# Kernel tuning notes

Hardware: AMD Instinct MI355X
Metric: run time of the kernel (lower is better)

## Reference

```python
import jax, jax.numpy as jnp
import numpy as np

# ---- static config (matches init_kwargs) ----
B, L, C = 32, 512, 32
PRED = 96
D = 256
PS, STRIDE = 16, 8
P = (L - PS) // STRIDE + 1  # 63 patches
H = 4
DH = D // H                 # 64 per head
K = 4                        # causal conv kernel size
NB = 2                       # num sLSTM blocks
UP = 384                     # round_up(1.3 * 256, 64) gated-FFN inner dim


def setup_inputs() -> dict:
    key = jax.random.key(0)
    ks = iter(jax.random.split(key, 32))
    def nrm(shape, s=0.02):
        return jax.random.normal(next(ks), shape, dtype=jnp.float32) * s
    f32 = jnp.float32
    return dict(
        x=jax.random.normal(next(ks), (B, L, C), dtype=f32),
        W_emb=nrm((PS, D)), b_emb=jnp.zeros((D,), f32),
        ln1_w=jnp.ones((NB, D), f32), ln1_b=jnp.zeros((NB, D), f32),
        conv_w=nrm((NB, K, D), 0.1), conv_b=jnp.zeros((NB, D), f32),
        Wg=nrm((NB, 4, H, DH, DH), 0.05),   # input gate projections (i,f,z,o), block-diag per head
        Rg=nrm((NB, 4, H, DH, DH), 0.05),   # recurrent kernels per head
        gb=jnp.zeros((NB, 4, D), f32),      # gate biases
        gn_w=jnp.ones((NB, D), f32),        # per-head groupnorm weight
        ln2_w=jnp.ones((NB, D), f32), ln2_b=jnp.zeros((NB, D), f32),
        up_w=nrm((NB, D, 2 * UP)), up_b=jnp.zeros((NB, 2 * UP), f32),
        dn_w=nrm((NB, UP, D)), dn_b=jnp.zeros((NB, D), f32),
        post_w=jnp.ones((D,), f32), post_b=jnp.zeros((D,), f32),
        W_proj=nrm((D * P, PRED)), b_proj=jnp.zeros((PRED,), f32),
    )


def _layernorm(x, w, b, eps=1e-5):
    mu = x.mean(-1, keepdims=True)
    var = x.var(-1, keepdims=True)
    return (x - mu) / jnp.sqrt(var + eps) * w + b


def _slstm_layer(x, conv_w, conv_b, Wg, Rg, gb, gn_w):
    # x: (N, S, D)
    N, S, _ = x.shape
    # causal depthwise conv (k=K) + swish -> feeds i,f gates
    xp = jnp.pad(x, ((0, 0), (K - 1, 0), (0, 0)))
    xc = sum(xp[:, k:k + S, :] * conv_w[k] for k in range(K)) + conv_b
    xc = xc * jax.nn.sigmoid(xc)
    xh = x.reshape(N, S, H, DH)
    xch = xc.reshape(N, S, H, DH)
    gi = jnp.einsum('nshd,hde->nshe', xch, Wg[0]) + gb[0].reshape(H, DH)
    gf = jnp.einsum('nshd,hde->nshe', xch, Wg[1]) + gb[1].reshape(H, DH)
    gz = jnp.einsum('nshd,hde->nshe', xh, Wg[2]) + gb[2].reshape(H, DH)
    go = jnp.einsum('nshd,hde->nshe', xh, Wg[3]) + gb[3].reshape(H, DH)
    gates = jnp.moveaxis(jnp.stack([gi, gf, gz, go], 0), 2, 0)  # (S, 4, N, H, DH)

    def step(carry, g):
        c, n, h, m = carry  # each (N, H, DH)
        rec = jnp.einsum('nhd,ghde->gnhe', h, Rg)  # (4, N, H, DH)
        ip, fp, zp, op = g[0] + rec[0], g[1] + rec[1], g[2] + rec[2], g[3] + rec[3]
        logf = m + jax.nn.log_sigmoid(fp)          # log(f_t) + m_{t-1}
        m_new = jnp.maximum(ip, logf)              # stabilizer
        i = jnp.exp(ip - m_new)
        f = jnp.exp(logf - m_new)
        c_new = f * c + i * jnp.tanh(zp)
        n_new = f * n + i
        h_new = jax.nn.sigmoid(op) * c_new / n_new
        return (c_new, n_new, h_new, m_new), h_new

    z0 = jnp.zeros((N, H, DH), x.dtype)
    _, hs = jax.lax.scan(step, (z0, z0, z0, z0), gates)
    y = jnp.moveaxis(hs, 0, 1)  # (N, S, H, DH)
    mu = y.mean(-1, keepdims=True)
    var = y.var(-1, keepdims=True)
    y = (y - mu) / jnp.sqrt(var + 1e-5)            # per-head groupnorm
    return y.reshape(N, S, D) * gn_w


def reference(x, W_emb, b_emb, ln1_w, ln1_b, conv_w, conv_b, Wg, Rg, gb, gn_w,
              ln2_w, ln2_b, up_w, up_b, dn_w, dn_b, post_w, post_b, W_proj, b_proj):
    Bb, Ll, Cc = x.shape
    xs = x.transpose(0, 2, 1).reshape(Bb * Cc, Ll)              # (N, L)
    idx = np.arange(P)[:, None] * STRIDE + np.arange(PS)[None, :]
    patches = xs[:, idx]                                         # (N, P, PS) unfold
    h = patches @ W_emb + b_emb                                  # (N, P, D)
    for blk in range(NB):
        h = h + _slstm_layer(_layernorm(h, ln1_w[blk], ln1_b[blk]),
                             conv_w[blk], conv_b[blk], Wg[blk], Rg[blk], gb[blk], gn_w[blk])
        u = _layernorm(h, ln2_w[blk], ln2_b[blk]) @ up_w[blk] + up_b[blk]
        g1, g2 = jnp.split(u, 2, axis=-1)
        h = h + (jax.nn.gelu(g1) * g2) @ dn_w[blk] + dn_b[blk]   # gated FFN
    h = _layernorm(h, post_w, post_b)                            # post-blocks norm
    out = h.reshape(Bb * Cc, D * P) @ W_proj + b_proj            # (N, PRED)
    return out.reshape(Bb, Cc, PRED).transpose(0, 2, 1)          # (B, PRED, C)
```

## Files before the change

### kernel.cpp

```cpp
#include <hip/hip_runtime.h>
#include <stdint.h>

typedef unsigned short u16;
typedef unsigned int   u32;
typedef __attribute__((ext_vector_type(8))) short bf16x8;
typedef __attribute__((ext_vector_type(4))) float f32x4;

#define NS      63
#define NSEQ    1024
#define DDIM    256
#define NHEAD   4
#define DHEAD   64
#define UPDIM   384
#define PREDN   96
#define LLEN    512
#define CCH     32
#define PSIZE   16
#define PSTRIDE 8
#define KC_PROJ 8
#define KCHUNK_PROJ 2016

__device__ __forceinline__ float bf2f(u32 lo16){
  union { u32 i; float f; } v; v.i = lo16 << 16; return v.f;
}
__device__ __forceinline__ float bf2f_hi(u32 u){
  union { u32 i; float f; } v; v.i = u & 0xffff0000u; return v.f;
}
__device__ __forceinline__ u16 f2bf(float f){
  union { u32 i; float f; } v; v.f = f;
  u32 u = v.i; u += 0x7fffu + ((u >> 16) & 1u);
  return (u16)(u >> 16);
}

__device__ __forceinline__ void gload16(const u16* g, u16* lds){
  __builtin_amdgcn_global_load_lds(
      (const __attribute__((address_space(1))) u32*)g,
      (__attribute__((address_space(3))) u32*)lds, 16, 0, 0);
}

template<int N> __device__ __forceinline__ void waitcnt_vm(){
  if constexpr (N == 0) asm volatile("s_waitcnt vmcnt(0)" ::: "memory");
  else if constexpr (N == 4) asm volatile("s_waitcnt vmcnt(4)" ::: "memory");
  else if constexpr (N == 6) asm volatile("s_waitcnt vmcnt(6)" ::: "memory");
}

__global__ __launch_bounds__(256) void cvt_transpose_t(
    const float* __restrict__ src, u16* __restrict__ dst, int R, int C){
  __shared__ u16 tile[32][33];
  int rb = blockIdx.x*32, cb = blockIdx.y*32;
  int tx = threadIdx.x & 31, ty = threadIdx.x >> 5;
  #pragma unroll
  for (int i = ty; i < 32; i += 8){
    int r = rb + i, c = cb + tx;
    tile[i][tx] = (r < R && c < C) ? f2bf(src[(size_t)r*C + c]) : (u16)0;
  }
  __syncthreads();
  #pragma unroll
  for (int i = ty; i < 32; i += 8){
    int c = cb + i, r = rb + tx;
    if (c < C && r < R) dst[(size_t)c*R + r] = tile[tx][i];
  }
}

__global__ __launch_bounds__(256) void cvt_gate(
    const float* __restrict__ src, u16* __restrict__ dst){
  int mat = blockIdx.x, t = threadIdx.x;
  const float* s = src + (size_t)mat*4096;
  u16* d = dst + (size_t)mat*4096;
  for (int i = t; i < 4096; i += 256){
    int r = i >> 6, c = i & 63;
    d[c*64 + r] = f2bf(s[i]);
  }
}

__global__ __launch_bounds__(256) void cvt_gateW2(
    const float* __restrict__ Wg, u16* __restrict__ dst){
  int mi = blockIdx.x;
  int blk = mi >> 3, p = (mi >> 2) & 1, hd = mi & 3;
  u16* d = dst + (size_t)mi*8192;
  for (int i = threadIdx.x; i < 8192; i += 256){
    int n = i >> 6, k = i & 63;
    int e = n >> 1, gl = n & 1;
    int g = 2*p + gl;
    d[i] = f2bf(Wg[((((size_t)blk*4 + g)*4 + hd)*64 + k)*64 + e]);
  }
}

__global__ __launch_bounds__(256) void patch_embed_ln_v(
    const float* __restrict__ x, const float* __restrict__ Wemb,
    const float* __restrict__ bemb, const float* __restrict__ w1,
    const float* __restrict__ b1, u16* __restrict__ h,
    u16* __restrict__ outA, int t_base){
  int wv = blockIdx.x*4 + (threadIdx.x >> 6);
  int lane = threadIdx.x & 63;
  int tg = t_base + wv;
  int n = tg / NS, s = tg - n*NS;
  int b = n >> 5, c = n & 31;
  int l0 = s * PSTRIDE;
  float4 acc = *(const float4*)(bemb + lane*4);
  #pragma unroll
  for (int p = 0; p < PSIZE; ++p){
    float xv = x[((size_t)b*LLEN + l0 + p)*CCH + c];
    float4 we = *(const float4*)(Wemb + p*DDIM + lane*4);
    acc.x += xv*we.x; acc.y += xv*we.y; acc.z += xv*we.z; acc.w += xv*we.w;
  }
  ushort4 hu; hu.x=f2bf(acc.x); hu.y=f2bf(acc.y); hu.z=f2bf(acc.z); hu.w=f2bf(acc.w);
  *(ushort4*)(h + (size_t)wv*DDIM + lane*4) = hu;
  float s1 = acc.x+acc.y+acc.z+acc.w;
  float s2 = acc.x*acc.x+acc.y*acc.y+acc.z*acc.z+acc.w*acc.w;
  #pragma unroll
  for (int o = 1; o < 64; o <<= 1){ s1 += __shfl_xor(s1,o,64); s2 += __shfl_xor(s2,o,64); }
  float mu = s1*(1.f/DDIM);
  float var = s2*(1.f/DDIM) - mu*mu;
  float rstd = rsqrtf(var + 1e-5f);
  float4 wf = *(const float4*)(w1 + lane*4);
  float4 bf = *(const float4*)(b1 + lane*4);
  ushort4 o4;
  o4.x = f2bf((acc.x-mu)*rstd*wf.x + bf.x);
  o4.y = f2bf((acc.y-mu)*rstd*wf.y + bf.y);
  o4.z = f2bf((acc.z-mu)*rstd*wf.z + bf.z);
  o4.w = f2bf((acc.w-mu)*rstd*wf.w + bf.w);
  *(ushort4*)(outA + (size_t)wv*DDIM + lane*4) = o4;
}

__global__ __launch_bounds__(256) void layernorm_v(
    const u16* __restrict__ in, const float* __restrict__ w,
    const float* __restrict__ b, u16* __restrict__ out){
  int wv = blockIdx.x*4 + (threadIdx.x >> 6);
  int lane = threadIdx.x & 63;
  ushort4 u = *(const ushort4*)(in + (size_t)wv*DDIM + lane*4);
  float v0=bf2f(u.x), v1=bf2f(u.y), v2=bf2f(u.z), v3=bf2f(u.w);
  float s1 = v0+v1+v2+v3, s2 = v0*v0+v1*v1+v2*v2+v3*v3;
  #pragma unroll
  for (int o = 1; o < 64; o <<= 1){ s1 += __shfl_xor(s1,o,64); s2 += __shfl_xor(s2,o,64); }
  float mu = s1*(1.f/DDIM);
  float var = s2*(1.f/DDIM) - mu*mu;
  float rstd = rsqrtf(var + 1e-5f);
  float4 wf = *(const float4*)(w + lane*4);
  float4 bf = *(const float4*)(b + lane*4);
  ushort4 o4;
  o4.x = f2bf((v0-mu)*rstd*wf.x + bf.x);
  o4.y = f2bf((v1-mu)*rstd*wf.y + bf.y);
  o4.z = f2bf((v2-mu)*rstd*wf.z + bf.z);
  o4.w = f2bf((v3-mu)*rstd*wf.w + bf.w);
  *(ushort4*)(out + (size_t)wv*DDIM + lane*4) = o4;
}

__global__ __launch_bounds__(256) void gn_res_ln_v(
    const u16* __restrict__ y, const float* __restrict__ gnw,
    const float* __restrict__ w2, const float* __restrict__ b2,
    u16* __restrict__ h, u16* __restrict__ outA){
  int wv = blockIdx.x*4 + (threadIdx.x >> 6);
  int lane = threadIdx.x & 63;
  ushort4 u = *(const ushort4*)(y + (size_t)wv*DDIM + lane*4);
  float v0=bf2f(u.x), v1=bf2f(u.y), v2=bf2f(u.z), v3=bf2f(u.w);
  float s1 = v0+v1+v2+v3, s2 = v0*v0+v1*v1+v2*v2+v3*v3;
  #pragma unroll
  for (int o = 1; o < 16; o <<= 1){ s1 += __shfl_xor(s1,o,64); s2 += __shfl_xor(s2,o,64); }
  float mu64 = s1*(1.f/64.f);
  float var64 = s2*(1.f/64.f) - mu64*mu64;
  float rstd64 = rsqrtf(var64 + 1e-5f);
  float4 gw = *(const float4*)(gnw + lane*4);
  ushort4 hu = *(const ushort4*)(h + (size_t)wv*DDIM + lane*4);
  float h0 = bf2f(hu.x) + (v0-mu64)*rstd64*gw.x;
  float h1 = bf2f(hu.y) + (v1-mu64)*rstd64*gw.y;
  float h2 = bf2f(hu.z) + (v2-mu64)*rstd64*gw.z;
  float h3 = bf2f(hu.w) + (v3-mu64)*rstd64*gw.w;
  ushort4 hn; hn.x=f2bf(h0); hn.y=f2bf(h1); hn.z=f2bf(h2); hn.w=f2bf(h3);
  *(ushort4*)(h + (size_t)wv*DDIM + lane*4) = hn;
  float t1 = h0+h1+h2+h3, t2 = h0*h0+h1*h1+h2*h2+h3*h3;
  #pragma unroll
  for (int o = 1; o < 64; o <<= 1){ t1 += __shfl_xor(t1,o,64); t2 += __shfl_xor(t2,o,64); }
  float mu = t1*(1.f/DDIM);
  float var = t2*(1.f/DDIM) - mu*mu;
  float rstd = rsqrtf(var + 1e-5f);
  float4 wf = *(const float4*)(w2 + lane*4);
  float4 bf = *(const float4*)(b2 + lane*4);
  ushort4 o4;
  o4.x = f2bf((h0-mu)*rstd*wf.x + bf.x);
  o4.y = f2bf((h1-mu)*rstd*wf.y + bf.y);
  o4.z = f2bf((h2-mu)*rstd*wf.z + bf.z);
  o4.w = f2bf((h3-mu)*rstd*wf.w + bf.w);
  *(ushort4*)(outA + (size_t)wv*DDIM + lane*4) = o4;
}

__global__ __launch_bounds__(256) void conv_silu_v(
    const u16* __restrict__ xln, const float* __restrict__ cw,
    const float* __restrict__ cb, u16* __restrict__ xc){
  int wv = blockIdx.x*4 + (threadIdx.x >> 6);
  int lane = threadIdx.x & 63;
  int s = wv % NS;
  float4 acc = *(const float4*)(cb + lane*4);
  #pragma unroll
  for (int k = 0; k < 4; ++k){
    int ss = s + k - 3;
    if (ss >= 0){
      ushort4 xu = *(const ushort4*)(xln + (size_t)(wv + k - 3)*DDIM + lane*4);
      float4 cv = *(const float4*)(cw + k*DDIM + lane*4);
      acc.x += bf2f(xu.x)*cv.x; acc.y += bf2f(xu.y)*cv.y;
      acc.z += bf2f(xu.z)*cv.z; acc.w += bf2f(xu.w)*cv.w;
    }
  }
  ushort4 o4;
  o4.x = f2bf(acc.x/(1.f + __expf(-acc.x)));
  o4.y = f2bf(acc.y/(1.f + __expf(-acc.y)));
  o4.z = f2bf(acc.z/(1.f + __expf(-acc.z)));
  o4.w = f2bf(acc.w/(1.f + __expf(-acc.w)));
  *(ushort4*)(xc + (size_t)wv*DDIM + lane*4) = o4;
}

template<int BM,int BN,int WR,int WC,int MR,int NR,int MODE,int VM>
__global__ __launch_bounds__(256) void mfma_gemm2(
    const u16* __restrict__ A, int lda,
    const u16* __restrict__ Wt, int ldwt,
    const float* __restrict__ bias, void* __restrict__ outp, int ldo,
    int ksteps, int kchunk, int Mtot)
{
  constexpr int nA = BM/16, nW = BN/16;
  __shared__ u16 As[2][BM*32];
  __shared__ u16 Ws[2][BN*32];
  const int tid = threadIdx.x;
  const int lane = tid & 63, wid = tid >> 6;
  const int wr = wid / WC, wc = wid % WC;
  const int fr = lane & 15, kb = lane >> 4;
  const int m0 = blockIdx.y*BM, n0 = blockIdx.x*BN;
  const int kc = blockIdx.z;
  const int kbeg = kc*kchunk;
  const u16* Ab = A + (size_t)m0*lda + kbeg;
  const u16* Wb = Wt + (size_t)n0*ldwt + kbeg;
  const int lrow = lane >> 2, lcol = (lane & 3)*8;

  auto stage = [&](int buf, int ks){
    int k0 = ks*32;
    for (int c = wid; c < nA; c += 4)
      gload16(Ab + (size_t)(c*16 + lrow)*lda + k0 + lcol, &As[buf][c*512]);
    for (int c = wid; c < nW; c += 4)
      gload16(Wb + (size_t)(c*16 + lrow)*ldwt + k0 + lcol, &Ws[buf][c*512]);
  };

  f32x4 acc[MR][NR];
  #pragma unroll
  for (int m=0;m<MR;++m)
    #pragma unroll
    for (int n=0;n<NR;++n) acc[m][n] = (f32x4){0.f,0.f,0.f,0.f};

  stage(0, 0);
  if (VM == 0) __syncthreads();
  int cur = 0;
  for (int ks = 0; ks < ksteps; ++ks){
    if (VM == 0){
      if (ks + 1 < ksteps) stage(cur^1, ks+1);
    } else {
      if (ks + 1 < ksteps){ stage(cur^1, ks+1); waitcnt_vm<VM>(); }
      else waitcnt_vm<0>();
      __builtin_amdgcn_s_barrier();
      asm volatile("" ::: "memory");
    }
    bf16x8 af[MR], wf[NR];
    #pragma unroll
    for (int m=0;m<MR;++m)
      af[m] = *(const bf16x8*)&As[cur][(wr*MR*16 + m*16 + fr)*32 + kb*8];
    #pragma unroll
    for (int n=0;n<NR;++n)
      wf[n] = *(const bf16x8*)&Ws[cur][(wc*NR*16 + n*16 + fr)*32 + kb*8];
    #pragma unroll
    for (int m=0;m<MR;++m)
      #pragma unroll
      for (int n=0;n<NR;++n)
        acc[m][n] = __builtin_amdgcn_mfma_f32_16x16x32_bf16(af[m], wf[n], acc[m][n], 0,0,0);
    if (VM == 0){
      __syncthreads();
    } else {
      asm volatile("" ::: "memory");
      __builtin_amdgcn_s_barrier();
    }
    cur ^= 1;
  }
  #pragma unroll
  for (int m=0;m<MR;++m){
    int rowb = m0 + wr*MR*16 + m*16 + kb*4;
    #pragma unroll
    for (int n=0;n<NR;++n){
      int col = n0 + wc*NR*16 + n*16 + fr;
      #pragma unroll
      for (int r=0;r<4;++r){
        int row = rowb + r;
        float v = acc[m][n][r];
        if (MODE == 1){
          u16* dst = (u16*)outp + (size_t)row*ldo + col;
          *dst = f2bf(bf2f(*dst) + v + bias[col]);
        } else {
          ((float*)outp)[((size_t)kc*Mtot + row)*ldo + col] = v;
        }
      }
    }
  }
}

__global__ __launch_bounds__(256) void mfma_gate2(
    const u16* __restrict__ xc, const u16* __restrict__ xh,
    const u16* __restrict__ Wg2, const float* __restrict__ gb,
    u16* __restrict__ gates)
{
  __shared__ u16 As[2][128*32];
  __shared__ u16 Ws[2][128*32];
  const int tid = threadIdx.x;
  const int lane = tid & 63, wid = tid >> 6;
  const int wr = wid >> 1, wc = wid & 1;
  const int fr = lane & 15, kb = lane >> 4;
  const int p = blockIdx.x >> 2, hd = blockIdx.x & 3;
  const int m0 = blockIdx.y*128;
  const u16* Ain = (p == 0) ? xc : xh;
  const u16* Wb = Wg2 + (size_t)blockIdx.x*8192;
  const int lrow = lane >> 2, lcol = (lane & 3)*8;

  auto stage = [&](int buf, int ks){
    int k0 = ks*32;
    for (int c = wid; c < 8; c += 4)
      gload16(Ain + (size_t)(m0 + c*16 + lrow)*DDIM + hd*64 + k0 + lcol, &As[buf][c*512]);
    for (int c = wid; c < 8; c += 4)
      gload16(Wb + (size_t)(c*16 + lrow)*64 + k0 + lcol, &Ws[buf][c*512]);
  };

  f32x4 acc[4][4];
  #pragma unroll
  for (int m=0;m<4;++m)
    #pragma unroll
    for (int n=0;n<4;++n) acc[m][n] = (f32x4){0.f,0.f,0.f,0.f};

  stage(0, 0);
  int cur = 0;
  #pragma unroll
  for (int ks = 0; ks < 2; ++ks){
    if (ks == 0){ stage(1, 1); waitcnt_vm<4>(); }
    else waitcnt_vm<0>();
    __builtin_amdgcn_s_barrier();
    asm volatile("" ::: "memory");
    bf16x8 af[4], wf[4];
    #pragma unroll
    for (int m=0;m<4;++m)
      af[m] = *(const bf16x8*)&As[cur][(wr*64 + m*16 + fr)*32 + kb*8];
    #pragma unroll
    for (int n=0;n<4;++n)
      wf[n] = *(const bf16x8*)&Ws[cur][(wc*64 + n*16 + fr)*32 + kb*8];
    #pragma unroll
    for (int m=0;m<4;++m)
      #pragma unroll
      for (int n=0;n<4;++n)
        acc[m][n] = __builtin_amdgcn_mfma_f32_16x16x32_bf16(af[m], wf[n], acc[m][n], 0,0,0);
    asm volatile("" ::: "memory");
    __builtin_amdgcn_s_barrier();
    cur ^= 1;
  }
  #pragma unroll
  for (int m=0;m<4;++m){
    int rowb = m0 + wr*64 + m*16 + kb*4;
    #pragma unroll
    for (int n=0;n<4;++n){
      int cl = wc*64 + n*16 + fr;
      int e = cl >> 1, gl = cl & 1;
      float bv = gb[(2*p + gl)*256 + hd*64 + e];
      int phys = hd*256 + p*128 + cl;
      #pragma unroll
      for (int r=0;r<4;++r)
        gates[(size_t)(rowb + r)*1024 + phys] = f2bf(acc[m][n][r] + bv);
    }
  }
}

__global__ __launch_bounds__(256) void mfma_up_gelu3(
    const u16* __restrict__ A, const u16* __restrict__ Wt,
    const float* __restrict__ ub, u16* __restrict__ gp)
{
  __shared__ u16 As[2][256*32];
  __shared__ u16 Ws[2][128*32];
  const int tid = threadIdx.x;
  const int lane = tid & 63, wid = tid >> 6;
  const int fr = lane & 15, kb = lane >> 4;
  const int m0 = blockIdx.y*256, n0 = blockIdx.x*64;
  const u16* W1 = Wt + (size_t)n0*256;
  const u16* W2 = Wt + (size_t)(384 + n0)*256;
  const int lrow = lane >> 2, lcol = (lane & 3)*8;

  auto stage = [&](int buf, int ks){
    int k0 = ks*32;
    for (int c = wid; c < 16; c += 4)
      gload16(A + (size_t)(m0 + c*16 + lrow)*256 + k0 + lcol, &As[buf][c*512]);
    for (int c = wid; c < 8; c += 4){
      const u16* src = (c < 4) ? (W1 + (size_t)(c*16 + lrow)*256)
                               : (W2 + (size_t)((c-4)*16 + lrow)*256);
      gload16(src + k0 + lcol, &Ws[buf][c*512]);
    }
  };

  f32x4 a1[4][4], a2[4][4];
  #pragma unroll
  for (int m=0;m<4;++m)
    #pragma unroll
    for (int n=0;n<4;++n){ a1[m][n]=(f32x4){0,0,0,0}; a2[m][n]=(f32x4){0,0,0,0}; }

  stage(0, 0);
  int cur = 0;
  #pragma unroll
  for (int ks = 0; ks < 8; ++ks){
    if (ks + 1 < 8){ stage(cur^1, ks+1); waitcnt_vm<6>(); }
    else waitcnt_vm<0>();
    __builtin_amdgcn_s_barrier();
    asm volatile("" ::: "memory");
    bf16x8 af[4], wf1[4], wf2[4];
    #pragma unroll
    for (int m=0;m<4;++m)
      af[m] = *(const bf16x8*)&As[cur][(wid*64 + m*16 + fr)*32 + kb*8];
    #pragma unroll
    for (int n=0;n<4;++n){
      wf1[n] = *(const bf16x8*)&Ws[cur][(n*16 + fr)*32 + kb*8];
      wf2[n] = *(const bf16x8*)&Ws[cur][(64 + n*16 + fr)*32 + kb*8];
    }
    #pragma unroll
    for (int m=0;m<4;++m)
      #pragma unroll
      for (int n=0;n<4;++n){
        a1[m][n] = __builtin_amdgcn_mfma_f32_16x16x32_bf16(af[m], wf1[n], a1[m][n], 0,0,0);
        a2[m][n] = __builtin_amdgcn_mfma_f32_16x16x32_bf16(af[m], wf2[n], a2[m][n], 0,0,0);
      }
    asm volatile("" ::: "memory");
    __builtin_amdgcn_s_barrier();
    cur ^= 1;
  }
  #pragma unroll
  for (int m=0;m<4;++m){
    int rowb = m0 + wid*64 + m*16 + kb*4;
    #pragma unroll
    for (int n=0;n<4;++n){
      int col = n0 + n*16 + fr;
      float b1 = ub[col], b2 = ub[384 + col];
      #pragma unroll
      for (int r=0;r<4;++r){
        float g1 = a1[m][n][r] + b1;
        float g2 = a2[m][n][r] + b2;
        float u  = 0.7978845608028654f*(g1 + 0.044715f*g1*g1*g1);
        float uc = fminf(fmaxf(u, -20.f), 20.f);
        float t2 = __expf(uc + uc);
        float th = (t2 - 1.f)/(t2 + 1.f);
        float ge = 0.5f*g1*(1.f + th);
        gp[(size_t)(rowb + r)*UPDIM + col] = f2bf(ge*g2);
      }
    }
  }
}

__global__ __launch_bounds__(256) void slstm_scan4(
    const u16* __restrict__ gates, const u16* __restrict__ Rgt,
    u16* __restrict__ y)
{
  __shared__ u16 h_lds[16*72];
  __shared__ float rec_lds[4][16][68];
  const int tid = threadIdx.x;
  const int w = tid >> 6, lane = tid & 63;
  const int hd = blockIdx.y, grp = blockIdx.x;
  const int fr = lane & 15, kb = lane >> 4;
  const int seq0 = grp*16;
  const u32* g32 = (const u32*)gates;

  bf16x8 bfr[4][2];
  {
    const u16* rb = Rgt + (size_t)(w*NHEAD + hd)*4096;
    #pragma unroll
    for (int n=0;n<4;++n)
      #pragma unroll
      for (int ks=0;ks<2;++ks)
        bfr[n][ks] = *(const bf16x8*)(rb + (size_t)(n*16 + fr)*64 + ks*32 + kb*8);
  }
  for (int i = tid; i < 16*72/2; i += 256) ((u32*)h_lds)[i] = 0u;
  float c[4]={0,0,0,0}, nst[4]={0,0,0,0}, m[4]={0,0,0,0};

  size_t gb4[4];
  #pragma unroll
  for (int si=0; si<4; ++si)
    gb4[si] = ((size_t)(seq0 + 4*w + si)*NS)*512 + hd*128 + lane;

  u32 g0[4][2], g1[4][2];
  #pragma unroll
  for (int si=0; si<4; ++si){
    g0[si][0] = g32[gb4[si]];        g0[si][1] = g32[gb4[si] + 64];
    g1[si][0] = g32[gb4[si] + 512];  g1[si][1] = g32[gb4[si] + 576];
  }
  __syncthreads();

  for (int s = 0; s < NS; ++s){
    u32 gn[4][2] = {};
    if (s + 2 < NS){
      #pragma unroll
      for (int si=0; si<4; ++si){
        size_t b2 = gb4[si] + (size_t)(s+2)*512;
        gn[si][0] = g32[b2];
        gn[si][1] = g32[b2 + 64];
      }
    }
    bf16x8 af0 = *(const bf16x8*)&h_lds[fr*72 + kb*8];
    bf16x8 af1 = *(const bf16x8*)&h_lds[fr*72 + 32 + kb*8];
    f32x4 acc[4];
    #pragma unroll
    for (int n=0;n<4;++n){
      acc[n] = (f32x4){0,0,0,0};
      acc[n] = __builtin_amdgcn_mfma_f32_16x16x32_bf16(af0, bfr[n][0], acc[n], 0,0,0);
      acc[n] = __builtin_amdgcn_mfma_f32_16x16x32_bf16(af1, bfr[n][1], acc[n], 0,0,0);
    }
    #pragma unroll
    for (int n=0;n<4;++n)
      #pragma unroll
      for (int r=0;r<4;++r)
        rec_lds[w][kb*4 + r][n*16 + fr] = acc[n][r];
    asm volatile("s_waitcnt lgkmcnt(0)" ::: "memory");
    __builtin_amdgcn_s_barrier();
    #pragma unroll
    for (int si=0; si<4; ++si){
      int sidx = 4*w + si;
      float ip = rec_lds[0][sidx][lane] + bf2f(g0[si][0] & 0xffffu);
      float fp = rec_lds[1][sidx][lane] + bf2f_hi(g0[si][0]);
      float zp = rec_lds[2][sidx][lane] + bf2f(g0[si][1] & 0xffffu);
      float op = rec_lds[3][sidx][lane] + bf2f_hi(g0[si][1]);
      float sp  = __logf(1.f + __expf(-fabsf(fp)));
      float lg  = m[si] + fminf(fp, 0.f) - sp;
      float mn  = fmaxf(ip, lg);
      float iv  = __expf(ip - mn);
      float fv  = __expf(lg - mn);
      float zz  = fminf(fabsf(zp), 15.f);
      float t2  = __expf(zz + zz);
      float tha = (t2 - 1.f)/(t2 + 1.f);
      float th  = (zp >= 0.f) ? tha : -tha;
      c[si]   = fv*c[si] + iv*th;
      nst[si] = fv*nst[si] + iv;
      m[si]   = mn;
      float hv = c[si] * __builtin_amdgcn_rcpf(nst[si]*(1.f + __expf(-op)));
      h_lds[sidx*72 + lane] = f2bf(hv);
      size_t t = (size_t)(seq0 + sidx)*NS + s;
      y[t*DDIM + hd*64 + lane] = f2bf(hv);
    }
    asm volatile("s_waitcnt lgkmcnt(0)" ::: "memory");
    __builtin_amdgcn_s_barrier();
    #pragma unroll
    for (int si=0; si<4; ++si){
      g0[si][0] = g1[si][0]; g0[si][1] = g1[si][1];
      g1[si][0] = gn[si][0]; g1[si][1] = gn[si][1];
    }
  }
}

__global__ __launch_bounds__(256) void proj_out(
    const float* __restrict__ ptmp, const float* __restrict__ bproj,
    float* __restrict__ out, int Nc, int n0glob){
  int gid = blockIdx.x*256 + threadIdx.x;
  if (gid >= Nc*PREDN) return;
  float acc = 0.f;
  #pragma unroll
  for (int kc = 0; kc < KC_PROJ; ++kc) acc += ptmp[(size_t)kc*Nc*PREDN + gid];
  int nl = gid / PREDN, j = gid - nl*PREDN;
  int n = n0glob + nl;
  out[((size_t)(n >> 5)*PREDN + j)*CCH + (n & 31)] = acc + bproj[j];
}

extern "C" void kernel_launch(void* const* d_in, const int* in_sizes, int n_in,
                              void* d_out, int out_size, void* d_ws, size_t ws_size,
                              hipStream_t stream) {
  const float* x      = (const float*)d_in[0];
  const float* W_emb  = (const float*)d_in[1];
  const float* b_emb  = (const float*)d_in[2];
  const float* ln1_w  = (const float*)d_in[3];
  const float* ln1_b  = (const float*)d_in[4];
  const float* conv_w = (const float*)d_in[5];
  const float* conv_b = (const float*)d_in[6];
  const float* Wg     = (const float*)d_in[7];
  const float* Rg     = (const float*)d_in[8];
  const float* gb     = (const float*)d_in[9];
  const float* gn_w   = (const float*)d_in[10];
  const float* ln2_w  = (const float*)d_in[11];
  const float* ln2_b  = (const float*)d_in[12];
  const float* up_w   = (const float*)d_in[13];
  const float* up_b   = (const float*)d_in[14];
  const float* dn_w   = (const float*)d_in[15];
  const float* dn_b   = (const float*)d_in[16];
  const float* post_w = (const float*)d_in[17];
  const float* post_b = (const float*)d_in[18];
  const float* W_proj = (const float*)d_in[19];
  const float* b_proj = (const float*)d_in[20];
  float* out = (float*)d_out;

  const size_t oWu   = 0;
  const size_t oWd   = 1572864;
  const size_t oWg2  = 2359296;
  const size_t oRgt  = 2621440;
  const size_t oWp   = 3145728;
  const size_t oChunk = 6242304;
  const size_t per_seq = (size_t)3584*NS;
  int Nc = 0;
  const int cands[3] = {1024, 512, 256};
  for (int i = 0; i < 3; ++i)
    if (oChunk + (size_t)cands[i]*per_seq <= ws_size){ Nc = cands[i]; break; }
  if (Nc == 0) return;

  char* wsb = (char*)d_ws;
  u16* Wu   = (u16*)(wsb + oWu);
  u16* Wd   = (u16*)(wsb + oWd);
  u16* Wg2  = (u16*)(wsb + oWg2);
  u16* Rgt  = (u16*)(wsb + oRgt);
  u16* Wtp  = (u16*)(wsb + oWp);

  for (int blk = 0; blk < 2; ++blk){
    cvt_transpose_t<<<dim3(8, 24), 256, 0, stream>>>(
        up_w + (size_t)blk*256*768, Wu + (size_t)blk*768*256, 256, 768);
    cvt_transpose_t<<<dim3(12, 8), 256, 0, stream>>>(
        dn_w + (size_t)blk*384*256, Wd + (size_t)blk*256*384, 384, 256);
  }
  cvt_gateW2<<<16, 256, 0, stream>>>(Wg, Wg2);
  cvt_gate<<<32, 256, 0, stream>>>(Rg, Rgt);
  cvt_transpose_t<<<dim3(504, 3), 256, 0, stream>>>(W_proj, Wtp, 16128, 96);

  for (int n0 = 0; n0 < NSEQ; n0 += Nc){
    const int    nc  = (NSEQ - n0 < Nc) ? (NSEQ - n0) : Nc;
    const size_t Tc  = (size_t)nc * NS;
    char* cb = wsb + oChunk;
    u16*   h_c   = (u16*)cb;
    u16*   bufA  = (u16*)(cb + Tc*512);
    u16*   bufB  = (u16*)(cb + Tc*1024);
    u16*   gates = (u16*)(cb + Tc*1536);
    u16*   gp    = gates;
    float* ptmp  = (float*)(cb + Tc*1536 + Tc*1024);
    const int t_base = n0*NS;
    const int Tci = (int)Tc;

    patch_embed_ln_v<<<Tci/4, 256, 0, stream>>>(
        x, W_emb, b_emb, ln1_w, ln1_b, h_c, bufA, t_base);

    for (int blk = 0; blk < 2; ++blk){
      if (blk == 1)
        layernorm_v<<<Tci/4, 256, 0, stream>>>(h_c, ln1_w + DDIM, ln1_b + DDIM, bufA);
      conv_silu_v<<<Tci/4, 256, 0, stream>>>(bufA, conv_w + blk*4*DDIM, conv_b + blk*DDIM, bufB);
      mfma_gate2<<<dim3(8, Tci/128), 256, 0, stream>>>(
          bufB, bufA, Wg2 + (size_t)blk*8*8192, gb + blk*4*DDIM, gates);
      slstm_scan4<<<dim3(nc/16, NHEAD), 256, 0, stream>>>(
          gates, Rgt + (size_t)blk*16*4096, bufB);
      gn_res_ln_v<<<Tci/4, 256, 0, stream>>>(
          bufB, gn_w + blk*DDIM, ln2_w + blk*DDIM, ln2_b + blk*DDIM, h_c, bufA);
      mfma_up_gelu3<<<dim3(6, Tci/256), 256, 0, stream>>>(
          bufA, Wu + (size_t)blk*768*256, up_b + blk*2*UPDIM, gp);
      mfma_gemm2<256,128,4,1,4,8,1,6><<<dim3(2, Tci/256), 256, 0, stream>>>(
          gp, UPDIM, Wd + (size_t)blk*256*384, UPDIM,
          dn_b + blk*DDIM, (void*)h_c, DDIM, 12, 0, 0);
    }

    layernorm_v<<<Tci/4, 256, 0, stream>>>(h_c, post_w, post_b, bufA);
    mfma_gemm2<64,96,2,2,2,3,2,0><<<dim3(1, nc/64, KC_PROJ), 256, 0, stream>>>(
        bufA, NS*DDIM, Wtp, NS*DDIM,
        b_proj, (void*)ptmp, PREDN, KCHUNK_PROJ/32, KCHUNK_PROJ, nc);
    proj_out<<<(nc*PREDN + 255)/256, 256, 0, stream>>>(ptmp, b_proj, out, nc, n0);
  }
}
```

Before: 760.1 us.

## XOR-swizzle LDS tiles and remap workgroups across XCDs in MFMA GEMMs

Applies an XOR swizzle to the 16-byte column chunks of the LDS A and W tiles in the generic GEMM, the gate GEMM and the up/GELU GEMM. The global source column is permuted at load time and the fragment reads undo the permutation, so the strided per-row bf16x8 reads no longer hit the same LDS banks. It also remaps the flat workgroup index so that neighbouring output tiles go to the same XCD, which should improve L2 reuse of shared A and W panels. The remap relies on round-robin dispatch of workgroups to 8 XCDs and adds some index arithmetic per block.

```diff
diff --git a/kernel.cpp b/kernel.cpp
--- a/kernel.cpp
+++ b/kernel.cpp
@@ -42,6 +42,17 @@
   if constexpr (N == 0) asm volatile("s_waitcnt vmcnt(0)" ::: "memory");
   else if constexpr (N == 4) asm volatile("s_waitcnt vmcnt(4)" ::: "memory");
   else if constexpr (N == 6) asm volatile("s_waitcnt vmcnt(6)" ::: "memory");
+}
+
+__device__ __forceinline__ void swz_tile(int &nt, int &mt){
+  int gx = gridDim.x, gy = gridDim.y;
+  int nwg = gx*gy;
+  int flat = blockIdx.y*gx + blockIdx.x;
+  int c = flat & 7, s = flat >> 3;
+  int q = nwg >> 3, r = nwg & 7;
+  int base = c*q + (c < r ? c : r);
+  int t = base + s;
+  nt = t % gx; mt = t / gx;
 }
 
 __global__ __launch_bounds__(256) void cvt_transpose_t(
@@ -223,12 +234,15 @@
   const int lane = tid & 63, wid = tid >> 6;
   const int wr = wid / WC, wc = wid % WC;
   const int fr = lane & 15, kb = lane >> 4;
-  const int m0 = blockIdx.y*BM, n0 = blockIdx.x*BN;
+  int nt, mt; swz_tile(nt, mt);
+  const int m0 = mt*BM, n0 = nt*BN;
   const int kc = blockIdx.z;
   const int kbeg = kc*kchunk;
   const u16* Ab = A + (size_t)m0*lda + kbeg;
   const u16* Wb = Wt + (size_t)n0*ldwt + kbeg;
-  const int lrow = lane >> 2, lcol = (lane & 3)*8;
+  const int lrow = lane >> 2;
+  const int lcol = (((lane & 3) ^ (lrow & 3)) * 8);
+  const int rsw = (kb ^ (fr & 3))*8;
 
   auto stage = [&](int buf, int ks){
     int k0 = ks*32;
@@ -259,10 +273,10 @@
     bf16x8 af[MR], wf[NR];
     #pragma unroll
     for (int m=0;m<MR;++m)
-      af[m] = *(const bf16x8*)&As[cur][(wr*MR*16 + m*16 + fr)*32 + kb*8];
+      af[m] = *(const bf16x8*)&As[cur][(wr*MR*16 + m*16 + fr)*32 + rsw];
     #pragma unroll
     for (int n=0;n<NR;++n)
-      wf[n] = *(const bf16x8*)&Ws[cur][(wc*NR*16 + n*16 + fr)*32 + kb*8];
+      wf[n] = *(const bf16x8*)&Ws[cur][(wc*NR*16 + n*16 + fr)*32 + rsw];
     #pragma unroll
     for (int m=0;m<MR;++m)
       #pragma unroll
@@ -308,11 +322,14 @@
   const int lane = tid & 63, wid = tid >> 6;
   const int wr = wid >> 1, wc = wid & 1;
   const int fr = lane & 15, kb = lane >> 4;
-  const int p = blockIdx.x >> 2, hd = blockIdx.x & 3;
-  const int m0 = blockIdx.y*128;
+  int nt, mt; swz_tile(nt, mt);
+  const int p = nt >> 2, hd = nt & 3;
+  const int m0 = mt*128;
   const u16* Ain = (p == 0) ? xc : xh;
-  const u16* Wb = Wg2 + (size_t)blockIdx.x*8192;
-  const int lrow = lane >> 2, lcol = (lane & 3)*8;
+  const u16* Wb = Wg2 + (size_t)nt*8192;
+  const int lrow = lane >> 2;
+  const int lcol = (((lane & 3) ^ (lrow & 3)) * 8);
+  const int rsw = (kb ^ (fr & 3))*8;
 
   auto stage = [&](int buf, int ks){
     int k0 = ks*32;
@@ -339,10 +356,10 @@
     bf16x8 af[4], wf[4];
     #pragma unroll
     for (int m=0;m<4;++m)
-      af[m] = *(const bf16x8*)&As[cur][(wr*64 + m*16 + fr)*32 + kb*8];
+      af[m] = *(const bf16x8*)&As[cur][(wr*64 + m*16 + fr)*32 + rsw];
     #pragma unroll
     for (int n=0;n<4;++n)
-      wf[n] = *(const bf16x8*)&Ws[cur][(wc*64 + n*16 + fr)*32 + kb*8];
+      wf[n] = *(const bf16x8*)&Ws[cur][(wc*64 + n*16 + fr)*32 + rsw];
     #pragma unroll
     for (int m=0;m<4;++m)
       #pragma unroll
@@ -377,10 +394,13 @@
   const int tid = threadIdx.x;
   const int lane = tid & 63, wid = tid >> 6;
   const int fr = lane & 15, kb = lane >> 4;
-  const int m0 = blockIdx.y*256, n0 = blockIdx.x*64;
+  int nt, mt; swz_tile(nt, mt);
+  const int m0 = mt*256, n0 = nt*64;
   const u16* W1 = Wt + (size_t)n0*256;
   const u16* W2 = Wt + (size_t)(384 + n0)*256;
-  const int lrow = lane >> 2, lcol = (lane & 3)*8;
+  const int lrow = lane >> 2;
+  const int lcol = (((lane & 3) ^ (lrow & 3)) * 8);
+  const int rsw = (kb ^ (fr & 3))*8;
 
   auto stage = [&](int buf, int ks){
     int k0 = ks*32;
@@ -410,11 +430,11 @@
     bf16x8 af[4], wf1[4], wf2[4];
     #pragma unroll
     for (int m=0;m<4;++m)
-      af[m] = *(const bf16x8*)&As[cur][(wid*64 + m*16 + fr)*32 + kb*8];
+      af[m] = *(const bf16x8*)&As[cur][(wid*64 + m*16 + fr)*32 + rsw];
     #pragma unroll
     for (int n=0;n<4;++n){
-      wf1[n] = *(const bf16x8*)&Ws[cur][(n*16 + fr)*32 + kb*8];
-      wf2[n] = *(const bf16x8*)&Ws[cur][(64 + n*16 + fr)*32 + kb*8];
+      wf1[n] = *(const bf16x8*)&Ws[cur][(n*16 + fr)*32 + rsw];
+      wf2[n] = *(const bf16x8*)&Ws[cur][(64 + n*16 + fr)*32 + rsw];
     }
     #pragma unroll
     for (int m=0;m<4;++m)
```

Result: faster. 731.9 us (-3.7%).
